# Optimization experiments

Measured on AMD Instinct MI355X. Metric: run time of the kernel, lower is better.

## Reference

```python
import jax, jax.numpy as jnp
import numpy as np

N = 8192
D = 64


def gcn_conv(x, edge_index, W, b):
    # PyG GCNConv: add self-loops, symmetric normalization, linear, aggregate.
    src, dst = edge_index[0], edge_index[1]
    loop = jnp.arange(x.shape[0])
    src = jnp.concatenate([src, loop])
    dst = jnp.concatenate([dst, loop])
    ones = jnp.ones(src.shape[0], dtype=x.dtype)
    deg = jax.ops.segment_sum(ones, dst, num_segments=x.shape[0])  # in-degree incl. self-loop
    dinv = jnp.where(deg > 0, jax.lax.rsqrt(deg), 0.0)
    norm = dinv[src] * dinv[dst]  # [E+N]
    h = x @ W  # [N, D]
    msg = norm[:, None] * h[src]  # gather + scale
    out = jax.ops.segment_sum(msg, dst, num_segments=x.shape[0])  # scatter-add
    return out + b


def setup_inputs() -> dict:
    key = jax.random.key(0)
    k1, k2, k3 = jax.random.split(key, 3)
    x = jax.random.normal(k1, (N, D), dtype=jnp.float32)
    edge_index = jax.random.randint(k2, (2, 32 * N), 0, N, dtype=jnp.int64)
    W = jax.random.normal(k3, (D, D), dtype=jnp.float32) / np.sqrt(D)
    b = jnp.zeros((D,), dtype=jnp.float32)
    return {"x": x, "edge_index": edge_index, "W": W, "b": b}


def reference(x, edge_index, W, b):
    h = jax.nn.relu(gcn_conv(x, edge_index, W, b))  # [N, D]
    return h @ h.T  # [N, N] reconstructed structure
```

## Files before the change

kernel.cpp:

```cpp
#include <hip/hip_runtime.h>
#include <hip/hip_bf16.h>

#define NN 8192
#define DD 64

typedef __attribute__((ext_vector_type(8))) short bf16x8;
typedef __attribute__((ext_vector_type(4))) float f32x4;

__global__ void k0_deg_init(int* __restrict__ deg) {
  int i = blockIdx.x * 256 + threadIdx.x;
  if (i < NN) deg[i] = 1;
}

__global__ void k1_degree(const int* __restrict__ dst, int E, int* __restrict__ deg) {
  int e = blockIdx.x * 256 + threadIdx.x;
  if (e < E) atomicAdd(&deg[dst[e]], 1);
}

__global__ void k2_scan(const int* __restrict__ deg, int* __restrict__ rowstart,
                        int* __restrict__ cursor, float* __restrict__ dinv) {
  __shared__ int part[256];
  int t = threadIdx.x;
  int base = t * 32;
  int loc[32];
  int s = 0;
#pragma unroll
  for (int i = 0; i < 32; i++) { loc[i] = s; s += deg[base + i] - 1; }
  part[t] = s;
  __syncthreads();
  for (int off = 1; off < 256; off <<= 1) {
    int u = (t >= off) ? part[t - off] : 0;
    __syncthreads();
    part[t] += u;
    __syncthreads();
  }
  int excl = (t == 0) ? 0 : part[t - 1];
#pragma unroll
  for (int i = 0; i < 32; i++) {
    int rs = excl + loc[i];
    rowstart[base + i] = rs;
    cursor[base + i] = rs;
    dinv[base + i] = rsqrtf((float)deg[base + i]);
  }
  if (t == 255) rowstart[NN] = excl + s;
}

__global__ void k3_fill(const int* __restrict__ src, const int* __restrict__ dst, int E,
                        int* __restrict__ cursor, int* __restrict__ csr) {
  int e = blockIdx.x * 256 + threadIdx.x;
  if (e < E) {
    int d = dst[e];
    int pos = atomicAdd(&cursor[d], 1);
    csr[pos] = src[e];
  }
}

__global__ void k4_xw(const float* __restrict__ x, const float* __restrict__ W,
                      float* __restrict__ h) {
  __shared__ float Wl[64 * 64];
  __shared__ float xl[4 * 64];
  int t = threadIdx.x;
#pragma unroll
  for (int i = 0; i < 16; i++) Wl[t + 256 * i] = W[t + 256 * i];
  int row0 = blockIdx.x * 4;
  xl[t] = x[row0 * 64 + t];
  __syncthreads();
  int r = t >> 6, d = t & 63;
  float acc = 0.f;
#pragma unroll
  for (int k = 0; k < 64; k++) acc += xl[r * 64 + k] * Wl[k * 64 + d];
  h[(row0 + r) * 64 + d] = acc;
}

__global__ void k5_agg(const float* __restrict__ h, const int* __restrict__ rowstart,
                       const int* __restrict__ csr, const float* __restrict__ dinv,
                       const float* __restrict__ b, unsigned short* __restrict__ hb) {
  int i = (blockIdx.x * 256 + threadIdx.x) >> 6;
  int lane = threadIdx.x & 63;
  float di = dinv[i];
  float acc = di * di * h[i * 64 + lane];
  int s0 = rowstart[i], s1 = rowstart[i + 1];
  for (int j = s0; j < s1; j++) {
    int s = csr[j];
    acc += di * dinv[s] * h[s * 64 + lane];
  }
  acc += b[lane];
  acc = fmaxf(acc, 0.f);
  __hip_bfloat16 bv = __float2bfloat16(acc);
  hb[i * 64 + lane] = *reinterpret_cast<unsigned short*>(&bv);
}

__global__ __launch_bounds__(256) void k6_gemm(const unsigned short* __restrict__ Hb,
                                               float* __restrict__ C) {
  int t = threadIdx.x;
  int w = t >> 6, lane = t & 63;
  int wm = w >> 1, wn = w & 1;
  int m0 = blockIdx.y * 128 + wm * 64;
  int n0 = blockIdx.x * 128 + wn * 64;
  int r = lane & 15, g = lane >> 4;

  bf16x8 a[4][2], bf[4][2];
#pragma unroll
  for (int mi = 0; mi < 4; mi++) {
#pragma unroll
    for (int s = 0; s < 2; s++) {
      a[mi][s] = *reinterpret_cast<const bf16x8*>(&Hb[(m0 + 16 * mi + r) * 64 + 32 * s + 8 * g]);
      bf[mi][s] = *reinterpret_cast<const bf16x8*>(&Hb[(n0 + 16 * mi + r) * 64 + 32 * s + 8 * g]);
    }
  }

  f32x4 acc[4][4];
#pragma unroll
  for (int mi = 0; mi < 4; mi++)
#pragma unroll
    for (int ni = 0; ni < 4; ni++) acc[mi][ni] = (f32x4){0.f, 0.f, 0.f, 0.f};

#pragma unroll
  for (int s = 0; s < 2; s++)
#pragma unroll
    for (int mi = 0; mi < 4; mi++)
#pragma unroll
      for (int ni = 0; ni < 4; ni++)
        acc[mi][ni] = __builtin_amdgcn_mfma_f32_16x16x32_bf16(bf[ni][s], a[mi][s],
                                                              acc[mi][ni], 0, 0, 0);

#pragma unroll
  for (int mi = 0; mi < 4; mi++) {
    int row = m0 + 16 * mi + r;
#pragma unroll
    for (int ni = 0; ni < 4; ni++) {
      *reinterpret_cast<f32x4*>(&C[row * NN + n0 + 16 * ni + 4 * g]) = acc[mi][ni];
    }
  }
}

extern "C" void kernel_launch(void* const* d_in, const int* in_sizes, int n_in,
                              void* d_out, int out_size, void* d_ws, size_t ws_size,
                              hipStream_t stream) {
  const float* x = (const float*)d_in[0];
  const int* ei = (const int*)d_in[1];
  const float* W = (const float*)d_in[2];
  const float* b = (const float*)d_in[3];
  float* C = (float*)d_out;
  int E = in_sizes[1] / 2;
  const int* src = ei;
  const int* dst = ei + E;

  char* ws = (char*)d_ws;
  int* deg       = (int*)(ws + 0);
  int* rowstart  = (int*)(ws + 32768);
  int* cursor    = (int*)(ws + 65792);
  float* dinv    = (float*)(ws + 98560);
  int* csr       = (int*)(ws + 131328);
  float* h       = (float*)(ws + 1179904);
  unsigned short* hb = (unsigned short*)(ws + 3277056);

  int eb = (E + 255) / 256;
  k0_deg_init<<<32, 256, 0, stream>>>(deg);
  k1_degree<<<eb, 256, 0, stream>>>(dst, E, deg);
  k2_scan<<<1, 256, 0, stream>>>(deg, rowstart, cursor, dinv);
  k3_fill<<<eb, 256, 0, stream>>>(src, dst, E, cursor, csr);
  k4_xw<<<NN / 4, 256, 0, stream>>>(x, W, h);
  k5_agg<<<NN / 4, 256, 0, stream>>>(h, rowstart, csr, dinv, b, hb);
  dim3 g(NN / 128, NN / 128);
  k6_gemm<<<g, 256, 0, stream>>>(hb, C);
}
```

Measured before the change: 342.7 us.

## Fuse aggregation with X·W by aggregating raw features before the linear transform

Because the aggregation is linear, the kernel now aggregates normalized neighbor rows of x first and then multiplies by W in the same kernel, removing the separate h buffer and one launch. The degree init kernel becomes a memset, and the self-loop count is added in the scan instead. Gathers read x rows in place of h rows at the same size, so the main saving is the h write/read round-trip and one launch. The fused block now loads W into shared memory for every 4-node block, as the old XW kernel already did.

```diff
diff --git a/kernel.cpp b/kernel.cpp
--- a/kernel.cpp
+++ b/kernel.cpp
@@ -6,11 +6,6 @@
 
 typedef __attribute__((ext_vector_type(8))) short bf16x8;
 typedef __attribute__((ext_vector_type(4))) float f32x4;
-
-__global__ void k0_deg_init(int* __restrict__ deg) {
-  int i = blockIdx.x * 256 + threadIdx.x;
-  if (i < NN) deg[i] = 1;
-}
 
 __global__ void k1_degree(const int* __restrict__ dst, int E, int* __restrict__ deg) {
   int e = blockIdx.x * 256 + threadIdx.x;
@@ -25,7 +20,7 @@
   int loc[32];
   int s = 0;
 #pragma unroll
-  for (int i = 0; i < 32; i++) { loc[i] = s; s += deg[base + i] - 1; }
+  for (int i = 0; i < 32; i++) { loc[i] = s; s += deg[base + i]; }
   part[t] = s;
   __syncthreads();
   for (int off = 1; off < 256; off <<= 1) {
@@ -40,7 +35,7 @@
     int rs = excl + loc[i];
     rowstart[base + i] = rs;
     cursor[base + i] = rs;
-    dinv[base + i] = rsqrtf((float)deg[base + i]);
+    dinv[base + i] = rsqrtf((float)(deg[base + i] + 1));
   }
   if (t == 255) rowstart[NN] = excl + s;
 }
@@ -55,39 +50,36 @@
   }
 }
 
-__global__ void k4_xw(const float* __restrict__ x, const float* __restrict__ W,
-                      float* __restrict__ h) {
+__global__ __launch_bounds__(256) void k45_agg_xw(
+    const float* __restrict__ x, const float* __restrict__ W,
+    const int* __restrict__ rowstart, const int* __restrict__ csr,
+    const float* __restrict__ dinv, const float* __restrict__ b,
+    unsigned short* __restrict__ hb) {
   __shared__ float Wl[64 * 64];
-  __shared__ float xl[4 * 64];
+  __shared__ float gl[4 * 64];
   int t = threadIdx.x;
 #pragma unroll
   for (int i = 0; i < 16; i++) Wl[t + 256 * i] = W[t + 256 * i];
-  int row0 = blockIdx.x * 4;
-  xl[t] = x[row0 * 64 + t];
+
+  int wave = t >> 6, lane = t & 63;
+  int node = blockIdx.x * 4 + wave;
+  float di = dinv[node];
+  float g = di * di * x[node * 64 + lane];
+  int s0 = rowstart[node], s1 = rowstart[node + 1];
+  for (int j = s0; j < s1; j++) {
+    int s = csr[j];
+    g += di * dinv[s] * x[s * 64 + lane];
+  }
+  gl[wave * 64 + lane] = g;
   __syncthreads();
-  int r = t >> 6, d = t & 63;
+
   float acc = 0.f;
 #pragma unroll
-  for (int k = 0; k < 64; k++) acc += xl[r * 64 + k] * Wl[k * 64 + d];
-  h[(row0 + r) * 64 + d] = acc;
-}
-
-__global__ void k5_agg(const float* __restrict__ h, const int* __restrict__ rowstart,
-                       const int* __restrict__ csr, const float* __restrict__ dinv,
-                       const float* __restrict__ b, unsigned short* __restrict__ hb) {
-  int i = (blockIdx.x * 256 + threadIdx.x) >> 6;
-  int lane = threadIdx.x & 63;
-  float di = dinv[i];
-  float acc = di * di * h[i * 64 + lane];
-  int s0 = rowstart[i], s1 = rowstart[i + 1];
-  for (int j = s0; j < s1; j++) {
-    int s = csr[j];
-    acc += di * dinv[s] * h[s * 64 + lane];
-  }
+  for (int k = 0; k < 64; k++) acc += gl[wave * 64 + k] * Wl[k * 64 + lane];
   acc += b[lane];
   acc = fmaxf(acc, 0.f);
   __hip_bfloat16 bv = __float2bfloat16(acc);
-  hb[i * 64 + lane] = *reinterpret_cast<unsigned short*>(&bv);
+  hb[node * 64 + lane] = *reinterpret_cast<unsigned short*>(&bv);
 }
 
 __global__ __launch_bounds__(256) void k6_gemm(const unsigned short* __restrict__ Hb,
@@ -152,16 +144,14 @@
   int* cursor    = (int*)(ws + 65792);
   float* dinv    = (float*)(ws + 98560);
   int* csr       = (int*)(ws + 131328);
-  float* h       = (float*)(ws + 1179904);
-  unsigned short* hb = (unsigned short*)(ws + 3277056);
+  unsigned short* hb = (unsigned short*)(ws + 1179904);
 
   int eb = (E + 255) / 256;
-  k0_deg_init<<<32, 256, 0, stream>>>(deg);
+  hipMemsetAsync(deg, 0, NN * sizeof(int), stream);
   k1_degree<<<eb, 256, 0, stream>>>(dst, E, deg);
   k2_scan<<<1, 256, 0, stream>>>(deg, rowstart, cursor, dinv);
   k3_fill<<<eb, 256, 0, stream>>>(src, dst, E, cursor, csr);
-  k4_xw<<<NN / 4, 256, 0, stream>>>(x, W, h);
-  k5_agg<<<NN / 4, 256, 0, stream>>>(h, rowstart, csr, dinv, b, hb);
+  k45_agg_xw<<<NN / 4, 256, 0, stream>>>(x, W, rowstart, csr, dinv, b, hb);
   dim3 g(NN / 128, NN / 128);
   k6_gemm<<<g, 256, 0, stream>>>(hb, C);
 }
```

Measured after the change: 336.4 us. About the same (-1.8%).
